# Optimization experiments

Measured on AMD Instinct MI355X. Metric: run time of the kernel, lower is better.

## Reference

```python
import jax, jax.numpy as jnp
import numpy as np

# dims (match init_kwargs / input_specs)
D = 768      # embed_dim
H = 12       # num query heads
G = 4        # num kv groups
E = 8        # num experts
K = 2        # experts per token
F = 4 * D    # ffn hidden dim
B, S, T = 2, 1024, 1024
DH = D // H  # head dim = 64
EPS = 1e-6


def setup_inputs() -> dict:
    key = jax.random.key(0)
    ks = jax.random.split(key, 16)

    def p(k, shape, scale=0.02):
        return jax.random.normal(k, shape, jnp.float32) * scale

    inp = {}
    inp['x'] = jax.random.normal(ks[0], (B, S, D), jnp.float32)
    inp['encoder_context'] = jax.random.normal(ks[1], (B, T, D), jnp.float32)
    for n in ('ln1', 'ln2', 'ln3'):
        inp[n + '_scale'] = jnp.ones((D,), jnp.float32)
        inp[n + '_bias'] = jnp.zeros((D,), jnp.float32)
    i = 2
    for pre in ('sa', 'ca'):
        inp[pre + '_wq'] = p(ks[i], (D, H * DH)); i += 1
        inp[pre + '_bq'] = jnp.zeros((H * DH,), jnp.float32)
        inp[pre + '_wk'] = p(ks[i], (D, G * DH)); i += 1
        inp[pre + '_bk'] = jnp.zeros((G * DH,), jnp.float32)
        inp[pre + '_wv'] = p(ks[i], (D, G * DH)); i += 1
        inp[pre + '_bv'] = jnp.zeros((G * DH,), jnp.float32)
        inp[pre + '_wo'] = p(ks[i], (H * DH, D)); i += 1
        inp[pre + '_bo'] = jnp.zeros((D,), jnp.float32)
    inp['gate_w'] = p(ks[i], (D, E)); i += 1
    inp['gate_b'] = jnp.zeros((E,), jnp.float32)
    inp['w1'] = p(ks[i], (E, D, F)); i += 1
    inp['b1'] = jnp.zeros((E, F), jnp.float32)
    inp['w2'] = p(ks[i], (E, F, D)); i += 1
    inp['b2'] = jnp.zeros((E, D), jnp.float32)
    return inp


def _ln(x, scale, bias):
    mu = jnp.mean(x, axis=-1, keepdims=True)
    var = jnp.mean(jnp.square(x - mu), axis=-1, keepdims=True)
    return (x - mu) * jax.lax.rsqrt(var + EPS) * scale + bias


def _gqa(q_in, kv_in, wq, bq, wk, bk, wv, bv, wo, bo, causal):
    Bq, Sq, _ = q_in.shape
    Skv = kv_in.shape[1]
    q = (q_in @ wq + bq).reshape(Bq, Sq, H, DH)
    k = (kv_in @ wk + bk).reshape(Bq, Skv, G, DH)
    v = (kv_in @ wv + bv).reshape(Bq, Skv, G, DH)
    rep = H // G
    k = jnp.repeat(k, rep, axis=2)  # [B,Skv,H,DH]
    v = jnp.repeat(v, rep, axis=2)
    scores = jnp.einsum('bqhd,bkhd->bhqk', q, k) / jnp.sqrt(jnp.asarray(DH, q.dtype))
    if causal:
        cmask = jnp.tril(jnp.ones((Sq, Skv), bool))
        scores = jnp.where(cmask[None, None], scores, jnp.finfo(scores.dtype).min)
    attn = jax.nn.softmax(scores, axis=-1)
    out = jnp.einsum('bhqk,bkhd->bqhd', attn, v).reshape(Bq, Sq, H * DH)
    return out @ wo + bo


def _moe(x, gate_w, gate_b, w1, b1, w2, b2):
    logits = x @ gate_w + gate_b                      # [B,S,E]
    probs = jax.nn.softmax(logits, axis=-1)
    top_v, top_i = jax.lax.top_k(probs, K)            # [B,S,K]
    top_v = top_v / jnp.sum(top_v, axis=-1, keepdims=True)
    combine = jnp.sum(jax.nn.one_hot(top_i, E, dtype=x.dtype) * top_v[..., None], axis=-2)  # [B,S,E]
    h = jax.nn.gelu(jnp.einsum('bsd,edf->ebsf', x, w1) + b1[:, None, None, :])
    y = jnp.einsum('ebsf,efd->ebsd', h, w2) + b2[:, None, None, :]
    return jnp.einsum('ebsd,bse->bsd', y, combine)


def reference(x, encoder_context,
              ln1_scale, ln1_bias, ln2_scale, ln2_bias, ln3_scale, ln3_bias,
              sa_wq, sa_bq, sa_wk, sa_bk, sa_wv, sa_bv, sa_wo, sa_bo,
              ca_wq, ca_bq, ca_wk, ca_bk, ca_wv, ca_bv, ca_wo, ca_bo,
              gate_w, gate_b, w1, b1, w2, b2):
    xn = _ln(x, ln1_scale, ln1_bias)
    x = x + _gqa(xn, xn, sa_wq, sa_bq, sa_wk, sa_bk, sa_wv, sa_bv, sa_wo, sa_bo, causal=True)
    xn = _ln(x, ln2_scale, ln2_bias)
    x = x + _gqa(xn, encoder_context, ca_wq, ca_bq, ca_wk, ca_bk, ca_wv, ca_bv, ca_wo, ca_bo, causal=False)
    xn = _ln(x, ln3_scale, ln3_bias)
    x = x + _moe(xn, gate_w, gate_b, w1, b1, w2, b2)
    return x
```

## Files before the change

### kernel.cpp

```cpp
#include <hip/hip_runtime.h>

#define DEV __device__ __forceinline__

typedef __attribute__((ext_vector_type(4))) float f32x4;
typedef __attribute__((ext_vector_type(8))) short short8;
typedef __attribute__((ext_vector_type(4))) unsigned int u32x4;
typedef __attribute__((ext_vector_type(4))) unsigned short us16x4;

#define D_ 768
#define S_ 1024
#define B_ 2
#define H_ 12
#define G_ 4
#define DH_ 64
#define E_ 8
#define F_ 3072
#define NTOK (B_*S_)

DEV unsigned short f2bf(float f){
  unsigned int b = __float_as_uint(f);
  b += 0x7FFFu + ((b >> 16) & 1u);
  return (unsigned short)(b >> 16);
}
DEV float bf2f(unsigned short h){ return __uint_as_float(((unsigned int)h) << 16); }
DEV unsigned int splitbf_pack(float v){
  unsigned short h = f2bf(v);
  unsigned short l = f2bf(v - bf2f(h));
  return (unsigned int)h | ((unsigned int)l << 16);
}

__global__ __launch_bounds__(256) void tcast_kernel(const float* __restrict__ W,
                                                    unsigned short* __restrict__ Wh,
                                                    unsigned short* __restrict__ Wl,
                                                    int K, int N){
  __shared__ float tile[32][33];
  long long zoff = (long long)blockIdx.z * K * N;
  const float* Wz = W + zoff;
  int n0 = blockIdx.x*32, k0 = blockIdx.y*32;
  int tx = threadIdx.x, ty = threadIdx.y;
  #pragma unroll
  for (int i=0;i<4;i++){
    int r = ty + i*8;
    tile[r][tx] = Wz[(long long)(k0+r)*N + n0 + tx];
  }
  __syncthreads();
  #pragma unroll
  for (int i=0;i<4;i++){
    int r = ty + i*8;
    float v = tile[tx][r];
    unsigned int hl = splitbf_pack(v);
    long long o = zoff + (long long)(n0+r)*K + k0 + tx;
    Wh[o] = (unsigned short)(hl & 0xFFFFu);
    if (Wl) Wl[o] = (unsigned short)(hl >> 16);
  }
}

__global__ __launch_bounds__(256) void ln_kernel(const float* __restrict__ x,
                                                 const float* __restrict__ sc,
                                                 const float* __restrict__ bi,
                                                 unsigned short* __restrict__ outb,
                                                 float* __restrict__ outf){
  __shared__ float red[8];
  long long row = blockIdx.x;
  const float* xr = x + row*D_;
  int tid = threadIdx.x;
  float v0 = xr[tid], v1 = xr[tid+256], v2 = xr[tid+512];
  float s = v0+v1+v2;
  float q = v0*v0 + v1*v1 + v2*v2;
  #pragma unroll
  for (int off=32; off; off>>=1){ s += __shfl_xor(s, off); q += __shfl_xor(q, off); }
  int lane = tid & 63, w = tid >> 6;
  if (lane == 0){ red[w] = s; red[4+w] = q; }
  __syncthreads();
  s = red[0]+red[1]+red[2]+red[3];
  q = red[4]+red[5]+red[6]+red[7];
  float mu  = s * (1.0f/D_);
  float var = q * (1.0f/D_) - mu*mu;
  float rstd = rsqrtf(var + 1e-6f);
  #pragma unroll
  for (int i=0;i<3;i++){
    int idx = tid + 256*i;
    float vv = (i==0) ? v0 : (i==1) ? v1 : v2;
    float o = (vv - mu)*rstd*sc[idx] + bi[idx];
    outf[row*D_ + idx] = o;
    if (outb) outb[row*D_ + idx] = f2bf(o);
  }
}

#define LDK 80
__global__ __launch_bounds__(256) void gemm_split(
    const float* __restrict__ A, int lda,
    const unsigned short* __restrict__ Wh,
    const unsigned short* __restrict__ Wl,
    const float* __restrict__ bias,
    const float* __restrict__ resid,
    float* __restrict__ Cf, int ldc,
    int K)
{
  __shared__ __align__(16) unsigned short Ash[64*LDK];
  __shared__ __align__(16) unsigned short Asl[64*LDK];
  __shared__ __align__(16) unsigned short Bsh[64*LDK];
  __shared__ __align__(16) unsigned short Bsl[64*LDK];
  const int r0 = blockIdx.y*64;
  const int n0 = blockIdx.x*64;
  const int tid = threadIdx.x;
  const int lane = tid & 63;
  const int wv = tid >> 6;
  const int wr = (wv>>1)*32, wc = (wv&1)*32;

  f32x4 acc[2][2];
  #pragma unroll
  for (int i=0;i<2;i++)
    #pragma unroll
    for (int j=0;j<2;j++) acc[i][j] = (f32x4){0.f,0.f,0.f,0.f};

  for (int k0 = 0; k0 < K; k0 += 64){
    #pragma unroll
    for (int i=0;i<2;i++){
      int c = tid + i*256;
      int rr = c >> 3;
      int kc = (c & 7) * 8;
      const float* ap = A + (long long)(r0+rr)*lda + k0 + kc;
      f32x4 a0 = *(const f32x4*)(ap);
      f32x4 a1 = *(const f32x4*)(ap + 4);
      unsigned int p0 = splitbf_pack(a0.x), p1 = splitbf_pack(a0.y);
      unsigned int p2 = splitbf_pack(a0.z), p3 = splitbf_pack(a0.w);
      unsigned int p4 = splitbf_pack(a1.x), p5 = splitbf_pack(a1.y);
      unsigned int p6 = splitbf_pack(a1.z), p7 = splitbf_pack(a1.w);
      us16x4 h0, h1, l0, l1;
      h0.x=(unsigned short)p0; l0.x=(unsigned short)(p0>>16);
      h0.y=(unsigned short)p1; l0.y=(unsigned short)(p1>>16);
      h0.z=(unsigned short)p2; l0.z=(unsigned short)(p2>>16);
      h0.w=(unsigned short)p3; l0.w=(unsigned short)(p3>>16);
      h1.x=(unsigned short)p4; l1.x=(unsigned short)(p4>>16);
      h1.y=(unsigned short)p5; l1.y=(unsigned short)(p5>>16);
      h1.z=(unsigned short)p6; l1.z=(unsigned short)(p6>>16);
      h1.w=(unsigned short)p7; l1.w=(unsigned short)(p7>>16);
      *(us16x4*)&Ash[rr*LDK + kc]     = h0;
      *(us16x4*)&Ash[rr*LDK + kc + 4] = h1;
      *(us16x4*)&Asl[rr*LDK + kc]     = l0;
      *(us16x4*)&Asl[rr*LDK + kc + 4] = l1;
      long long bo = (long long)(n0+rr)*K + k0 + kc;
      *(u32x4*)&Bsh[rr*LDK + kc] = *(const u32x4*)(Wh + bo);
      *(u32x4*)&Bsl[rr*LDK + kc] = *(const u32x4*)(Wl + bo);
    }
    __syncthreads();
    #pragma unroll
    for (int ks=0; ks<2; ks++){
      int koff = ks*32 + (lane>>4)*8;
      short8 ah0 = *(const short8*)&Ash[(wr +      (lane&15))*LDK + koff];
      short8 ah1 = *(const short8*)&Ash[(wr + 16 + (lane&15))*LDK + koff];
      short8 al0 = *(const short8*)&Asl[(wr +      (lane&15))*LDK + koff];
      short8 al1 = *(const short8*)&Asl[(wr + 16 + (lane&15))*LDK + koff];
      short8 bh0 = *(const short8*)&Bsh[(wc +      (lane&15))*LDK + koff];
      short8 bh1 = *(const short8*)&Bsh[(wc + 16 + (lane&15))*LDK + koff];
      short8 bl0 = *(const short8*)&Bsl[(wc +      (lane&15))*LDK + koff];
      short8 bl1 = *(const short8*)&Bsl[(wc + 16 + (lane&15))*LDK + koff];
      acc[0][0] = __builtin_amdgcn_mfma_f32_16x16x32_bf16(ah0, bh0, acc[0][0], 0,0,0);
      acc[0][1] = __builtin_amdgcn_mfma_f32_16x16x32_bf16(ah0, bh1, acc[0][1], 0,0,0);
      acc[1][0] = __builtin_amdgcn_mfma_f32_16x16x32_bf16(ah1, bh0, acc[1][0], 0,0,0);
      acc[1][1] = __builtin_amdgcn_mfma_f32_16x16x32_bf16(ah1, bh1, acc[1][1], 0,0,0);
      acc[0][0] = __builtin_amdgcn_mfma_f32_16x16x32_bf16(ah0, bl0, acc[0][0], 0,0,0);
      acc[0][1] = __builtin_amdgcn_mfma_f32_16x16x32_bf16(ah0, bl1, acc[0][1], 0,0,0);
      acc[1][0] = __builtin_amdgcn_mfma_f32_16x16x32_bf16(ah1, bl0, acc[1][0], 0,0,0);
      acc[1][1] = __builtin_amdgcn_mfma_f32_16x16x32_bf16(ah1, bl1, acc[1][1], 0,0,0);
      acc[0][0] = __builtin_amdgcn_mfma_f32_16x16x32_bf16(al0, bh0, acc[0][0], 0,0,0);
      acc[0][1] = __builtin_amdgcn_mfma_f32_16x16x32_bf16(al0, bh1, acc[0][1], 0,0,0);
      acc[1][0] = __builtin_amdgcn_mfma_f32_16x16x32_bf16(al1, bh0, acc[1][0], 0,0,0);
      acc[1][1] = __builtin_amdgcn_mfma_f32_16x16x32_bf16(al1, bh1, acc[1][1], 0,0,0);
    }
    __syncthreads();
  }

  #pragma unroll
  for (int fi=0; fi<2; fi++)
  #pragma unroll
  for (int fj=0; fj<2; fj++)
  #pragma unroll
  for (int reg=0; reg<4; reg++){
    int r = r0 + wr + fi*16 + (lane>>4)*4 + reg;
    int col = n0 + wc + fj*16 + (lane&15);
    float val = acc[fi][fj][reg] + bias[col];
    if (resid) val += resid[(long long)r*ldc + col];
    Cf[(long long)r*ldc + col] = val;
  }
}

__global__ __launch_bounds__(256) void gemm_nt(
    const unsigned short* __restrict__ A, int lda,
    const unsigned short* __restrict__ Wt, long long wstride,
    const float* __restrict__ bias, int bias_stride,
    const int* __restrict__ counts,
    const int* __restrict__ a_idx, int a_idx_stride,
    const int* __restrict__ row_base,
    float* __restrict__ Cf, unsigned short* __restrict__ Cb, int ldc,
    int M, int K, int do_gelu)
{
  __shared__ __align__(16) unsigned short As[64*LDK];
  __shared__ __align__(16) unsigned short Bs[64*LDK];
  const int z = blockIdx.z;
  const int Mz = counts ? counts[z] : M;
  const int r0 = blockIdx.y*64;
  if (r0 >= Mz) return;
  const int n0 = blockIdx.x*64;
  const int obase = row_base ? row_base[z] : 0;
  const unsigned short* Wz = Wt + (long long)z*wstride;
  const float* bz = bias + (long long)z*bias_stride;
  const int tid = threadIdx.x;
  const int lane = tid & 63;
  const int wv = tid >> 6;
  const int wr = (wv>>1)*32, wc = (wv&1)*32;

  long long arow[2];
  #pragma unroll
  for (int i=0;i<2;i++){
    int c = tid + i*256;
    int rr = c >> 3;
    int r = r0 + rr;
    int rcl = (r < Mz) ? r : (Mz-1);
    arow[i] = a_idx ? (long long)a_idx[(long long)z*a_idx_stride + rcl]
                    : (long long)(obase + rcl);
  }

  f32x4 acc[2][2];
  #pragma unroll
  for (int i=0;i<2;i++)
    #pragma unroll
    for (int j=0;j<2;j++) acc[i][j] = (f32x4){0.f,0.f,0.f,0.f};

  for (int k0 = 0; k0 < K; k0 += 64){
    #pragma unroll
    for (int i=0;i<2;i++){
      int c = tid + i*256;
      int rr = c >> 3;
      int kc = (c & 7) * 8;
      *(u32x4*)&As[rr*LDK + kc] = *(const u32x4*)(A + arow[i]*lda + k0 + kc);
      *(u32x4*)&Bs[rr*LDK + kc] = *(const u32x4*)(Wz + (long long)(n0+rr)*K + k0 + kc);
    }
    __syncthreads();
    #pragma unroll
    for (int ks=0; ks<2; ks++){
      int koff = ks*32 + (lane>>4)*8;
      short8 a0 = *(const short8*)&As[(wr +      (lane&15))*LDK + koff];
      short8 a1 = *(const short8*)&As[(wr + 16 + (lane&15))*LDK + koff];
      short8 b0 = *(const short8*)&Bs[(wc +      (lane&15))*LDK + koff];
      short8 b1 = *(const short8*)&Bs[(wc + 16 + (lane&15))*LDK + koff];
      acc[0][0] = __builtin_amdgcn_mfma_f32_16x16x32_bf16(a0, b0, acc[0][0], 0,0,0);
      acc[0][1] = __builtin_amdgcn_mfma_f32_16x16x32_bf16(a0, b1, acc[0][1], 0,0,0);
      acc[1][0] = __builtin_amdgcn_mfma_f32_16x16x32_bf16(a1, b0, acc[1][0], 0,0,0);
      acc[1][1] = __builtin_amdgcn_mfma_f32_16x16x32_bf16(a1, b1, acc[1][1], 0,0,0);
    }
    __syncthreads();
  }

  #pragma unroll
  for (int fi=0; fi<2; fi++)
  #pragma unroll
  for (int fj=0; fj<2; fj++)
  #pragma unroll
  for (int reg=0; reg<4; reg++){
    int ml = wr + fi*16 + (lane>>4)*4 + reg;
    int r = r0 + ml;
    if (r >= Mz) continue;
    int col = n0 + wc + fj*16 + (lane&15);
    float val = acc[fi][fj][reg] + bz[col];
    if (do_gelu){
      float xx = val;
      float t = tanhf(0.7978845608028654f*(xx + 0.044715f*xx*xx*xx));
      val = 0.5f*xx*(1.0f + t);
    }
    long long orow = (long long)obase + r;
    if (Cf) Cf[orow*ldc + col] = val;
    if (Cb) Cb[orow*ldc + col] = f2bf(val);
  }
}

__global__ __launch_bounds__(256) void kv_split_kernel(const float* __restrict__ in,
                                                       unsigned short* __restrict__ hi,
                                                       unsigned short* __restrict__ lo,
                                                       int n4){
  int i = blockIdx.x*256 + threadIdx.x;
  if (i >= n4) return;
  f32x4 v = *(const f32x4*)(in + (long long)i*4);
  unsigned int p0 = splitbf_pack(v.x), p1 = splitbf_pack(v.y);
  unsigned int p2 = splitbf_pack(v.z), p3 = splitbf_pack(v.w);
  us16x4 h, l;
  h.x=(unsigned short)p0; l.x=(unsigned short)(p0>>16);
  h.y=(unsigned short)p1; l.y=(unsigned short)(p1>>16);
  h.z=(unsigned short)p2; l.z=(unsigned short)(p2>>16);
  h.w=(unsigned short)p3; l.w=(unsigned short)(p3>>16);
  *(us16x4*)(hi + (long long)i*4) = h;
  *(us16x4*)(lo + (long long)i*4) = l;
}

__global__ __launch_bounds__(256) void vt_split_kernel(const float* __restrict__ vin,
                                                       unsigned short* __restrict__ vth,
                                                       unsigned short* __restrict__ vtl){
  __shared__ float tile[32][33];
  int s0 = blockIdx.x*32, d0 = blockIdx.y*32;
  int bg = blockIdx.z; int b = bg >> 2, g = bg & 3;
  int tx = threadIdx.x, ty = threadIdx.y;
  #pragma unroll
  for (int i=0;i<4;i++){
    int r = ty + i*8;
    tile[r][tx] = vin[(long long)(b*1024 + s0 + r)*256 + g*64 + d0 + tx];
  }
  __syncthreads();
  #pragma unroll
  for (int i=0;i<4;i++){
    int d = d0 + ty + i*8;
    unsigned int pk = splitbf_pack(tile[tx][ty + i*8]);
    long long o = (long long)(bg*64 + d)*1024 + s0 + tx;
    vth[o] = (unsigned short)(pk & 0xFFFFu);
    vtl[o] = (unsigned short)(pk >> 16);
  }
}

#define AT_LDK 72
#define AT_LDP 76
__global__ __launch_bounds__(256, 2) void attn_mfma(
    const float* __restrict__ q,
    const unsigned short* __restrict__ kh, const unsigned short* __restrict__ kl,
    const unsigned short* __restrict__ vth, const unsigned short* __restrict__ vtl,
    float* __restrict__ ctx, int causal)
{
  __shared__ __align__(16) unsigned short KhS[64*AT_LDK];
  __shared__ __align__(16) unsigned short KlS[64*AT_LDK];
  __shared__ __align__(16) unsigned short VhS[64*AT_LDK];
  __shared__ __align__(16) unsigned short VlS[64*AT_LDK];
  __shared__ __align__(16) unsigned int   Pp[4][16*AT_LDP];

  const int qblk = blockIdx.x;
  const int h = blockIdx.y;
  const int b = blockIdx.z;
  const int g = h / (H_/G_);
  const int tid = threadIdx.x;
  const int lane = tid & 63;
  const int w = tid >> 6;
  const int l15 = lane & 15;
  const int l4 = lane >> 4;
  const int qb0 = qblk*64;

  short8 qh[2], ql[2];
  #pragma unroll
  for (int ks=0; ks<2; ks++){
    const float* qp = q + ((long long)(b*S_ + qb0 + w*16 + l15))*D_ + h*DH_ + ks*32 + l4*8;
    f32x4 q0 = *(const f32x4*)qp;
    f32x4 q1 = *(const f32x4*)(qp + 4);
    float qq[8] = {q0.x,q0.y,q0.z,q0.w,q1.x,q1.y,q1.z,q1.w};
    #pragma unroll
    for (int j=0;j<8;j++){
      unsigned int pk = splitbf_pack(qq[j]*0.125f);
      qh[ks][j] = (short)(pk & 0xFFFFu);
      ql[ks][j] = (short)(pk >> 16);
    }
  }

  f32x4 o[4];
  #pragma unroll
  for (int fd=0; fd<4; fd++) o[fd] = (f32x4){0.f,0.f,0.f,0.f};
  float m[4]    = {-3.0e38f,-3.0e38f,-3.0e38f,-3.0e38f};
  float lsum[4] = {0.f,0.f,0.f,0.f};

  const int ntiles = causal ? (qblk + 1) : (S_/64);
  for (int kt=0; kt<ntiles; kt++){
    __syncthreads();
    {
      int r = tid >> 2, c = tid & 3;
      long long krow = (long long)(b*S_ + kt*64 + r)*(G_*DH_) + g*DH_;
      long long vrow = (long long)((b*G_ + g)*64 + r)*S_ + kt*64;
      *(u32x4*)&KhS[r*AT_LDK + c*8]     = *(const u32x4*)(kh + krow + c*8);
      *(u32x4*)&KhS[r*AT_LDK + (c+4)*8] = *(const u32x4*)(kh + krow + (c+4)*8);
      *(u32x4*)&KlS[r*AT_LDK + c*8]     = *(const u32x4*)(kl + krow + c*8);
      *(u32x4*)&KlS[r*AT_LDK + (c+4)*8] = *(const u32x4*)(kl + krow + (c+4)*8);
      *(u32x4*)&VhS[r*AT_LDK + c*8]     = *(const u32x4*)(vth + vrow + c*8);
      *(u32x4*)&VhS[r*AT_LDK + (c+4)*8] = *(const u32x4*)(vth + vrow + (c+4)*8);
      *(u32x4*)&VlS[r*AT_LDK + c*8]     = *(const u32x4*)(vtl + vrow + c*8);
      *(u32x4*)&VlS[r*AT_LDK + (c+4)*8] = *(const u32x4*)(vtl + vrow + (c+4)*8);
    }
// ... 56 lines not shown
      ps += __shfl_xor(ps, 4); ps += __shfl_xor(ps, 8);
      lsum[reg] = lsum[reg]*c[reg] + ps;
      o[0][reg] *= c[reg]; o[1][reg] *= c[reg];
      o[2][reg] *= c[reg]; o[3][reg] *= c[reg];
    }

    #pragma unroll
    for (int ks=0; ks<2; ks++){
      u32x4 pa = *(const u32x4*)&Pp[w][l15*AT_LDP + ks*32 + l4*8];
      u32x4 pb = *(const u32x4*)&Pp[w][l15*AT_LDP + ks*32 + l4*8 + 4];
      short8 ph, pl;
      #pragma unroll
      for (int j=0;j<4;j++){
        ph[j]   = (short)(pa[j] & 0xFFFFu); pl[j]   = (short)(pa[j] >> 16);
        ph[4+j] = (short)(pb[j] & 0xFFFFu); pl[4+j] = (short)(pb[j] >> 16);
      }
      #pragma unroll
      for (int fd=0; fd<4; fd++){
        short8 vh = *(const short8*)&VhS[(fd*16 + l15)*AT_LDK + ks*32 + l4*8];
        short8 vl = *(const short8*)&VlS[(fd*16 + l15)*AT_LDK + ks*32 + l4*8];
        o[fd] = __builtin_amdgcn_mfma_f32_16x16x32_bf16(ph, vh, o[fd], 0,0,0);
        o[fd] = __builtin_amdgcn_mfma_f32_16x16x32_bf16(pl, vh, o[fd], 0,0,0);
        o[fd] = __builtin_amdgcn_mfma_f32_16x16x32_bf16(ph, vl, o[fd], 0,0,0);
      }
    }
  }

  #pragma unroll
  for (int reg=0; reg<4; reg++){
    float inv = 1.0f / lsum[reg];
    long long tok = b*S_ + qb0 + w*16 + l4*4 + reg;
    #pragma unroll
    for (int fd=0; fd<4; fd++){
      ctx[tok*D_ + h*DH_ + fd*16 + l15] = o[fd][reg]*inv;
    }
  }
}

__global__ __launch_bounds__(256) void gate_kernel(const float* __restrict__ xnf,
                                                   const float* __restrict__ gw,
                                                   const float* __restrict__ gb,
                                                   int* __restrict__ counts,
                                                   int* __restrict__ toklist,
                                                   int* __restrict__ route_e,
                                                   int* __restrict__ route_pos,
                                                   float* __restrict__ route_w){
  int t = blockIdx.x*4 + (threadIdx.x >> 6);
  int lane = threadIdx.x & 63;
  float acc[E_];
  #pragma unroll
  for (int e=0;e<E_;e++) acc[e] = 0.f;
  #pragma unroll
  for (int i=0;i<12;i++){
    int d = lane + 64*i;
    float xv = xnf[(long long)t*D_ + d];
    const float* w = gw + (long long)d*E_;
    #pragma unroll
    for (int e=0;e<E_;e++) acc[e] += xv*w[e];
  }
  #pragma unroll
  for (int off=32; off; off>>=1)
    #pragma unroll
    for (int e=0;e<E_;e++) acc[e] += __shfl_xor(acc[e], off);
  if (lane == 0){
    #pragma unroll
    for (int e=0;e<E_;e++) acc[e] += gb[e];
    int e0 = 0;
// ... 53 lines not shown
  const float* ln2b  = (const float*)d_in[5];
  const float* ln3s  = (const float*)d_in[6];
  const float* ln3b  = (const float*)d_in[7];
  const float* sa_wq = (const float*)d_in[8];
  const float* sa_bq = (const float*)d_in[9];
  const float* sa_wk = (const float*)d_in[10];
  const float* sa_bk = (const float*)d_in[11];
  const float* sa_wv = (const float*)d_in[12];
  const float* sa_bv = (const float*)d_in[13];
  const float* sa_wo = (const float*)d_in[14];
  const float* sa_bo = (const float*)d_in[15];
  const float* ca_wq = (const float*)d_in[16];
  const float* ca_bq = (const float*)d_in[17];
  const float* ca_wk = (const float*)d_in[18];
  const float* ca_bk = (const float*)d_in[19];
  const float* ca_wv = (const float*)d_in[20];
  const float* ca_bv = (const float*)d_in[21];
  const float* ca_wo = (const float*)d_in[22];
  const float* ca_bo = (const float*)d_in[23];
  const float* gate_w= (const float*)d_in[24];
  const float* gate_b= (const float*)d_in[25];
  const float* w1    = (const float*)d_in[26];
  const float* b1    = (const float*)d_in[27];
  const float* w2    = (const float*)d_in[28];
  const float* b2    = (const float*)d_in[29];
  float* out = (float*)d_out;

  char* p = (char*)d_ws;
  auto alloc = [&](size_t bytes)->void*{
    void* r = (void*)p;
    p += (bytes + 255) & ~(size_t)255;
    return r;
  };
  unsigned short* wqh_sa = (unsigned short*)alloc((size_t)D_*D_*2);
  unsigned short* wql_sa = (unsigned short*)alloc((size_t)D_*D_*2);
  unsigned short* wkh_sa = (unsigned short*)alloc((size_t)D_*G_*DH_*2);
  unsigned short* wkl_sa = (unsigned short*)alloc((size_t)D_*G_*DH_*2);
  unsigned short* wvh_sa = (unsigned short*)alloc((size_t)D_*G_*DH_*2);
  unsigned short* wvl_sa = (unsigned short*)alloc((size_t)D_*G_*DH_*2);
  unsigned short* woh_sa = (unsigned short*)alloc((size_t)D_*D_*2);
  unsigned short* wol_sa = (unsigned short*)alloc((size_t)D_*D_*2);
  unsigned short* wqh_ca = (unsigned short*)alloc((size_t)D_*D_*2);
  unsigned short* wql_ca = (unsigned short*)alloc((size_t)D_*D_*2);
  unsigned short* wkh_ca = (unsigned short*)alloc((size_t)D_*G_*DH_*2);
  unsigned short* wkl_ca = (unsigned short*)alloc((size_t)D_*G_*DH_*2);
  unsigned short* wvh_ca = (unsigned short*)alloc((size_t)D_*G_*DH_*2);
  unsigned short* wvl_ca = (unsigned short*)alloc((size_t)D_*G_*DH_*2);
  unsigned short* woh_ca = (unsigned short*)alloc((size_t)D_*D_*2);
  unsigned short* wol_ca = (unsigned short*)alloc((size_t)D_*D_*2);
  unsigned short* w1T = (unsigned short*)alloc((size_t)E_*D_*F_*2);
  unsigned short* w2T = (unsigned short*)alloc((size_t)E_*D_*F_*2);
  unsigned short* xn_b = (unsigned short*)alloc((size_t)NTOK*D_*2);
  unsigned short* hbuf = (unsigned short*)alloc((size_t)2*NTOK*F_*2);
  unsigned short* khp = (unsigned short*)alloc((size_t)NTOK*G_*DH_*2);
  unsigned short* klp = (unsigned short*)alloc((size_t)NTOK*G_*DH_*2);
  unsigned short* vtp_h = (unsigned short*)alloc((size_t)NTOK*G_*DH_*2);
  unsigned short* vtp_l = (unsigned short*)alloc((size_t)NTOK*G_*DH_*2);
  float* xnf  = (float*)alloc((size_t)NTOK*D_*4);
  float* qbuf = (float*)alloc((size_t)NTOK*D_*4);
  float* kbuf = (float*)alloc((size_t)NTOK*G_*DH_*4);
  float* vbuf = (float*)alloc((size_t)NTOK*G_*DH_*4);
  float* ctx  = (float*)alloc((size_t)NTOK*D_*4);
  float* xbuf = (float*)alloc((size_t)NTOK*D_*4);
  float* ybuf = (float*)alloc((size_t)2*NTOK*D_*4);
  int* counts    = (int*)alloc(E_*4);
  int* offs      = (int*)alloc(E_*4);
  int* toklist   = (int*)alloc((size_t)E_*NTOK*4);
  int* route_e   = (int*)alloc((size_t)2*NTOK*4);
  int* route_pos = (int*)alloc((size_t)2*NTOK*4);
  float* route_w = (float*)alloc((size_t)2*NTOK*4);

  (void)hipMemsetAsync(counts, 0, E_*sizeof(int), stream);

  dim3 tb(32,8);
  tcast_kernel<<<dim3(24,24,1), tb, 0, stream>>>(sa_wq, wqh_sa, wql_sa, 768, 768);
  tcast_kernel<<<dim3( 8,24,1), tb, 0, stream>>>(sa_wk, wkh_sa, wkl_sa, 768, 256);
  tcast_kernel<<<dim3( 8,24,1), tb, 0, stream>>>(sa_wv, wvh_sa, wvl_sa, 768, 256);
  tcast_kernel<<<dim3(24,24,1), tb, 0, stream>>>(sa_wo, woh_sa, wol_sa, 768, 768);
  tcast_kernel<<<dim3(24,24,1), tb, 0, stream>>>(ca_wq, wqh_ca, wql_ca, 768, 768);
  tcast_kernel<<<dim3( 8,24,1), tb, 0, stream>>>(ca_wk, wkh_ca, wkl_ca, 768, 256);
  tcast_kernel<<<dim3( 8,24,1), tb, 0, stream>>>(ca_wv, wvh_ca, wvl_ca, 768, 256);
  tcast_kernel<<<dim3(24,24,1), tb, 0, stream>>>(ca_wo, woh_ca, wol_ca, 768, 768);
  tcast_kernel<<<dim3(96,24,E_), tb, 0, stream>>>(w1, w1T, nullptr, 768, 3072);
  tcast_kernel<<<dim3(24,96,E_), tb, 0, stream>>>(w2, w2T, nullptr, 3072, 768);

  ln_kernel<<<NTOK, 256, 0, stream>>>(x, ln1s, ln1b, nullptr, xnf);
  gemm_split<<<dim3(12,32), 256, 0, stream>>>(xnf, 768, wqh_sa, wql_sa, sa_bq, nullptr, qbuf, 768, 768);
  gemm_split<<<dim3( 4,32), 256, 0, stream>>>(xnf, 768, wkh_sa, wkl_sa, sa_bk, nullptr, kbuf, 256, 768);
  gemm_split<<<dim3( 4,32), 256, 0, stream>>>(xnf, 768, wvh_sa, wvl_sa, sa_bv, nullptr, vbuf, 256, 768);
  kv_split_kernel<<<dim3(NTOK*G_*DH_/4/256), 256, 0, stream>>>(kbuf, khp, klp, NTOK*G_*DH_/4);
  vt_split_kernel<<<dim3(32,2,8), tb, 0, stream>>>(vbuf, vtp_h, vtp_l);
  attn_mfma<<<dim3(16,12,2), 256, 0, stream>>>(qbuf, khp, klp, vtp_h, vtp_l, ctx, 1);
  gemm_split<<<dim3(12,32), 256, 0, stream>>>(ctx, 768, woh_sa, wol_sa, sa_bo, x, xbuf, 768, 768);

  ln_kernel<<<NTOK, 256, 0, stream>>>(xbuf, ln2s, ln2b, nullptr, xnf);
  gemm_split<<<dim3(12,32), 256, 0, stream>>>(xnf, 768, wqh_ca, wql_ca, ca_bq, nullptr, qbuf, 768, 768);
  gemm_split<<<dim3( 4,32), 256, 0, stream>>>(enc, 768, wkh_ca, wkl_ca, ca_bk, nullptr, kbuf, 256, 768);
  gemm_split<<<dim3( 4,32), 256, 0, stream>>>(enc, 768, wvh_ca, wvl_ca, ca_bv, nullptr, vbuf, 256, 768);
  kv_split_kernel<<<dim3(NTOK*G_*DH_/4/256), 256, 0, stream>>>(kbuf, khp, klp, NTOK*G_*DH_/4);
  vt_split_kernel<<<dim3(32,2,8), tb, 0, stream>>>(vbuf, vtp_h, vtp_l);
  attn_mfma<<<dim3(16,12,2), 256, 0, stream>>>(qbuf, khp, klp, vtp_h, vtp_l, ctx, 0);
  gemm_split<<<dim3(12,32), 256, 0, stream>>>(ctx, 768, woh_ca, wol_ca, ca_bo, xbuf, xbuf, 768, 768);

  ln_kernel<<<NTOK, 256, 0, stream>>>(xbuf, ln3s, ln3b, xn_b, xnf);
  gate_kernel<<<NTOK/4, 256, 0, stream>>>(xnf, gate_w, gate_b,
      counts, toklist, route_e, route_pos, route_w);
  offsets_kernel<<<1, 64, 0, stream>>>(counts, offs);
  gemm_nt<<<dim3(48,32,E_), 256, 0, stream>>>(xn_b, 768, w1T, (long long)F_*D_, b1, F_,
      counts, toklist, NTOK, offs, nullptr, hbuf, F_, NTOK, 768, 1);
  gemm_nt<<<dim3(12,32,E_), 256, 0, stream>>>(hbuf, F_, w2T, (long long)F_*D_, b2, D_,
      counts, nullptr, 0, offs, ybuf, nullptr, 768, NTOK, F_, 0);
  combine_kernel<<<NTOK, 192, 0, stream>>>(xbuf, ybuf, route_e, route_pos, route_w, offs, out);
}
```

Measured before the change: 537.3 us.

## Fuse QKV projections, pre-split activations, and enlarge GEMM tiles to 128

Concatenates the self-attention Q/K/V weights and the cross-attention K/V weights so each group is one GEMM launch. LayerNorm and attention now emit hi/lo bf16 splits directly, so the GEMMs load pre-split operands instead of converting fp32 in the inner loop. The split GEMM tiles grow to 128 rows and the MoE GEMMs to 128x128, which raises reuse per load but lowers block count and occupancy. Several conversion kernels are removed, and a few small bias-concat and encoder-split kernels are added.

```diff
diff --git a/kernel.cpp b/kernel.cpp
--- a/kernel.cpp
+++ b/kernel.cpp
@@ -55,10 +55,37 @@
   }
 }
 
+__global__ void split_rows(const float* __restrict__ in, int ld, int width,
+                           unsigned short* __restrict__ hi, unsigned short* __restrict__ lo){
+  long long t = blockIdx.x;
+  int c = threadIdx.x*4;
+  f32x4 v = *(const f32x4*)(in + t*ld + c);
+  unsigned int p0 = splitbf_pack(v.x), p1 = splitbf_pack(v.y);
+  unsigned int p2 = splitbf_pack(v.z), p3 = splitbf_pack(v.w);
+  us16x4 h, l;
+  h.x=(unsigned short)p0; l.x=(unsigned short)(p0>>16);
+  h.y=(unsigned short)p1; l.y=(unsigned short)(p1>>16);
+  h.z=(unsigned short)p2; l.z=(unsigned short)(p2>>16);
+  h.w=(unsigned short)p3; l.w=(unsigned short)(p3>>16);
+  *(us16x4*)(hi + t*width + c) = h;
+  *(us16x4*)(lo + t*width + c) = l;
+}
+
+__global__ void concat_bias(const float* __restrict__ b0, int n0,
+                            const float* __restrict__ b1, int n1,
+                            const float* __restrict__ b2, int n2,
+                            float* __restrict__ out){
+  int i = blockIdx.x*256 + threadIdx.x;
+  if (i < n0) out[i] = b0[i];
+  else if (i < n0+n1) out[i] = b1[i-n0];
+  else if (i < n0+n1+n2) out[i] = b2[i-n0-n1];
+}
+
 __global__ __launch_bounds__(256) void ln_kernel(const float* __restrict__ x,
                                                  const float* __restrict__ sc,
                                                  const float* __restrict__ bi,
-                                                 unsigned short* __restrict__ outb,
+                                                 unsigned short* __restrict__ outh,
+                                                 unsigned short* __restrict__ outl,
                                                  float* __restrict__ outf){
   __shared__ float red[8];
   long long row = blockIdx.x;
@@ -82,111 +109,96 @@
     int idx = tid + 256*i;
     float vv = (i==0) ? v0 : (i==1) ? v1 : v2;
     float o = (vv - mu)*rstd*sc[idx] + bi[idx];
-    outf[row*D_ + idx] = o;
-    if (outb) outb[row*D_ + idx] = f2bf(o);
+    unsigned int pk = splitbf_pack(o);
+    outh[row*D_ + idx] = (unsigned short)(pk & 0xFFFFu);
+    if (outl) outl[row*D_ + idx] = (unsigned short)(pk >> 16);
+    if (outf) outf[row*D_ + idx] = o;
   }
 }
 
 #define LDK 80
-__global__ __launch_bounds__(256) void gemm_split(
-    const float* __restrict__ A, int lda,
-    const unsigned short* __restrict__ Wh,
-    const unsigned short* __restrict__ Wl,
+__global__ __launch_bounds__(256) void gemm3(
+    const unsigned short* __restrict__ Ah, const unsigned short* __restrict__ Al, int lda,
+    const unsigned short* __restrict__ Wh, const unsigned short* __restrict__ Wl, int K,
     const float* __restrict__ bias,
-    const float* __restrict__ resid,
-    float* __restrict__ Cf, int ldc,
-    int K)
+    const float* __restrict__ resid, int ldr,
+    float* __restrict__ Cf, int ldc)
 {
-  __shared__ __align__(16) unsigned short Ash[64*LDK];
-  __shared__ __align__(16) unsigned short Asl[64*LDK];
-  __shared__ __align__(16) unsigned short Bsh[64*LDK];
-  __shared__ __align__(16) unsigned short Bsl[64*LDK];
-  const int r0 = blockIdx.y*64;
+  __shared__ __align__(16) unsigned short AshH[128*LDK];
+  __shared__ __align__(16) unsigned short AshL[128*LDK];
+  __shared__ __align__(16) unsigned short BshH[64*LDK];
+  __shared__ __align__(16) unsigned short BshL[64*LDK];
+  const int r0 = blockIdx.y*128;
   const int n0 = blockIdx.x*64;
   const int tid = threadIdx.x;
   const int lane = tid & 63;
   const int wv = tid >> 6;
-  const int wr = (wv>>1)*32, wc = (wv&1)*32;
-
-  f32x4 acc[2][2];
-  #pragma unroll
-  for (int i=0;i<2;i++)
+  const int wr = (wv>>1)*64, wc = (wv&1)*32;
+  const int l15 = lane & 15, l4 = lane >> 4;
+
+  f32x4 acc[4][2];
+  #pragma unroll
+  for (int i=0;i<4;i++)
     #pragma unroll
     for (int j=0;j<2;j++) acc[i][j] = (f32x4){0.f,0.f,0.f,0.f};
 
   for (int k0 = 0; k0 < K; k0 += 64){
+    #pragma unroll
+    for (int i=0;i<4;i++){
+      int c = tid + i*256;
+      int rr = c >> 3, kc = (c & 7)*8;
+      long long src = (long long)(r0+rr)*lda + k0 + kc;
+      *(u32x4*)&AshH[rr*LDK+kc] = *(const u32x4*)(Ah + src);
+      *(u32x4*)&AshL[rr*LDK+kc] = *(const u32x4*)(Al + src);
+    }
     #pragma unroll
     for (int i=0;i<2;i++){
       int c = tid + i*256;
-      int rr = c >> 3;
-      int kc = (c & 7) * 8;
-      const float* ap = A + (long long)(r0+rr)*lda + k0 + kc;
-      f32x4 a0 = *(const f32x4*)(ap);
-      f32x4 a1 = *(const f32x4*)(ap + 4);
-      unsigned int p0 = splitbf_pack(a0.x), p1 = splitbf_pack(a0.y);
-      unsigned int p2 = splitbf_pack(a0.z), p3 = splitbf_pack(a0.w);
-      unsigned int p4 = splitbf_pack(a1.x), p5 = splitbf_pack(a1.y);
-      unsigned int p6 = splitbf_pack(a1.z), p7 = splitbf_pack(a1.w);
-      us16x4 h0, h1, l0, l1;
-      h0.x=(unsigned short)p0; l0.x=(unsigned short)(p0>>16);
-      h0.y=(unsigned short)p1; l0.y=(unsigned short)(p1>>16);
-      h0.z=(unsigned short)p2; l0.z=(unsigned short)(p2>>16);
-      h0.w=(unsigned short)p3; l0.w=(unsigned short)(p3>>16);
-      h1.x=(unsigned short)p4; l1.x=(unsigned short)(p4>>16);
-      h1.y=(unsigned short)p5; l1.y=(unsigned short)(p5>>16);
-      h1.z=(unsigned short)p6; l1.z=(unsigned short)(p6>>16);
-      h1.w=(unsigned short)p7; l1.w=(unsigned short)(p7>>16);
-      *(us16x4*)&Ash[rr*LDK + kc]     = h0;
-      *(us16x4*)&Ash[rr*LDK + kc + 4] = h1;
-      *(us16x4*)&Asl[rr*LDK + kc]     = l0;
-      *(us16x4*)&Asl[rr*LDK + kc + 4] = l1;
-      long long bo = (long long)(n0+rr)*K + k0 + kc;
-      *(u32x4*)&Bsh[rr*LDK + kc] = *(const u32x4*)(Wh + bo);
-      *(u32x4*)&Bsl[rr*LDK + kc] = *(const u32x4*)(Wl + bo);
+      int rr = c >> 3, kc = (c & 7)*8;
+      long long src = (long long)(n0+rr)*K + k0 + kc;
+      *(u32x4*)&BshH[rr*LDK+kc] = *(const u32x4*)(Wh + src);
+      *(u32x4*)&BshL[rr*LDK+kc] = *(const u32x4*)(Wl + src);
     }
     __syncthreads();
     #pragma unroll
     for (int ks=0; ks<2; ks++){
-      int koff = ks*32 + (lane>>4)*8;
-      short8 ah0 = *(const short8*)&Ash[(wr +      (lane&15))*LDK + koff];
-      short8 ah1 = *(const short8*)&Ash[(wr + 16 + (lane&15))*LDK + koff];
-      short8 al0 = *(const short8*)&Asl[(wr +      (lane&15))*LDK + koff];
-      short8 al1 = *(const short8*)&Asl[(wr + 16 + (lane&15))*LDK + koff];
-      short8 bh0 = *(const short8*)&Bsh[(wc +      (lane&15))*LDK + koff];
-      short8 bh1 = *(const short8*)&Bsh[(wc + 16 + (lane&15))*LDK + koff];
-      short8 bl0 = *(const short8*)&Bsl[(wc +      (lane&15))*LDK + koff];
-      short8 bl1 = *(const short8*)&Bsl[(wc + 16 + (lane&15))*LDK + koff];
-      acc[0][0] = __builtin_amdgcn_mfma_f32_16x16x32_bf16(ah0, bh0, acc[0][0], 0,0,0);
-      acc[0][1] = __builtin_amdgcn_mfma_f32_16x16x32_bf16(ah0, bh1, acc[0][1], 0,0,0);
-      acc[1][0] = __builtin_amdgcn_mfma_f32_16x16x32_bf16(ah1, bh0, acc[1][0], 0,0,0);
-      acc[1][1] = __builtin_amdgcn_mfma_f32_16x16x32_bf16(ah1, bh1, acc[1][1], 0,0,0);
-      acc[0][0] = __builtin_amdgcn_mfma_f32_16x16x32_bf16(ah0, bl0, acc[0][0], 0,0,0);
-      acc[0][1] = __builtin_amdgcn_mfma_f32_16x16x32_bf16(ah0, bl1, acc[0][1], 0,0,0);
-      acc[1][0] = __builtin_amdgcn_mfma_f32_16x16x32_bf16(ah1, bl0, acc[1][0], 0,0,0);
-      acc[1][1] = __builtin_amdgcn_mfma_f32_16x16x32_bf16(ah1, bl1, acc[1][1], 0,0,0);
-      acc[0][0] = __builtin_amdgcn_mfma_f32_16x16x32_bf16(al0, bh0, acc[0][0], 0,0,0);
-      acc[0][1] = __builtin_amdgcn_mfma_f32_16x16x32_bf16(al0, bh1, acc[0][1], 0,0,0);
-      acc[1][0] = __builtin_amdgcn_mfma_f32_16x16x32_bf16(al1, bh0, acc[1][0], 0,0,0);
-      acc[1][1] = __builtin_amdgcn_mfma_f32_16x16x32_bf16(al1, bh1, acc[1][1], 0,0,0);
+      int koff = ks*32 + l4*8;
+      short8 bh[2], bl[2];
+      #pragma unroll
+      for (int fj=0; fj<2; fj++){
+        bh[fj] = *(const short8*)&BshH[(wc + fj*16 + l15)*LDK + koff];
+        bl[fj] = *(const short8*)&BshL[(wc + fj*16 + l15)*LDK + koff];
+      }
+      #pragma unroll
+      for (int fi=0; fi<4; fi++){
+        short8 ah = *(const short8*)&AshH[(wr + fi*16 + l15)*LDK + koff];
+        short8 al = *(const short8*)&AshL[(wr + fi*16 + l15)*LDK + koff];
+        #pragma unroll
+        for (int fj=0; fj<2; fj++){
+          acc[fi][fj] = __builtin_amdgcn_mfma_f32_16x16x32_bf16(ah, bh[fj], acc[fi][fj], 0,0,0);
+          acc[fi][fj] = __builtin_amdgcn_mfma_f32_16x16x32_bf16(al, bh[fj], acc[fi][fj], 0,0,0);
+          acc[fi][fj] = __builtin_amdgcn_mfma_f32_16x16x32_bf16(ah, bl[fj], acc[fi][fj], 0,0,0);
+        }
+      }
     }
     __syncthreads();
   }
 
   #pragma unroll
-  for (int fi=0; fi<2; fi++)
+  for (int fi=0; fi<4; fi++)
   #pragma unroll
   for (int fj=0; fj<2; fj++)
   #pragma unroll
   for (int reg=0; reg<4; reg++){
-    int r = r0 + wr + fi*16 + (lane>>4)*4 + reg;
-    int col = n0 + wc + fj*16 + (lane&15);
+    int r = r0 + wr + fi*16 + l4*4 + reg;
+    int col = n0 + wc + fj*16 + l15;
     float val = acc[fi][fj][reg] + bias[col];
-    if (resid) val += resid[(long long)r*ldc + col];
+    if (resid) val += resid[(long long)r*ldr + col];
     Cf[(long long)r*ldc + col] = val;
   }
 }
 
-__global__ __launch_bounds__(256) void gemm_nt(
+__global__ __launch_bounds__(256) void gemm_nt128(
     const unsigned short* __restrict__ A, int lda,
     const unsigned short* __restrict__ Wt, long long wstride,
     const float* __restrict__ bias, int bias_stride,
@@ -194,26 +206,27 @@
     const int* __restrict__ a_idx, int a_idx_stride,
     const int* __restrict__ row_base,
     float* __restrict__ Cf, unsigned short* __restrict__ Cb, int ldc,
-    int M, int K, int do_gelu)
+    int K, int do_gelu)
 {
-  __shared__ __align__(16) unsigned short As[64*LDK];
-  __shared__ __align__(16) unsigned short Bs[64*LDK];
+  __shared__ __align__(16) unsigned short As[128*LDK];
+  __shared__ __align__(16) unsigned short Bs[128*LDK];
   const int z = blockIdx.z;
-  const int Mz = counts ? counts[z] : M;
-  const int r0 = blockIdx.y*64;
+  const int Mz = counts[z];
+  const int r0 = blockIdx.y*128;
   if (r0 >= Mz) return;
-  const int n0 = blockIdx.x*64;
-  const int obase = row_base ? row_base[z] : 0;
+  const int n0 = blockIdx.x*128;
+  const int obase = row_base[z];
   const unsigned short* Wz = Wt + (long long)z*wstride;
   const float* bz = bias + (long long)z*bias_stride;
   const int tid = threadIdx.x;
   const int lane = tid & 63;
   const int wv = tid >> 6;
-  const int wr = (wv>>1)*32, wc = (wv&1)*32;
-
-  long long arow[2];
-  #pragma unroll
-  for (int i=0;i<2;i++){
+  const int wr = (wv>>1)*64, wc = (wv&1)*64;
+  const int l15 = lane & 15, l4 = lane >> 4;
+
+  long long arow[4];
+  #pragma unroll
+  for (int i=0;i<4;i++){
     int c = tid + i*256;
     int rr = c >> 3;
     int r = r0 + rr;
@@ -222,47 +235,48 @@
                     : (long long)(obase + rcl);
   }
 
-  f32x4 acc[2][2];
-  #pragma unroll
-  for (int i=0;i<2;i++)
-    #pragma unroll
-    for (int j=0;j<2;j++) acc[i][j] = (f32x4){0.f,0.f,0.f,0.f};
+  f32x4 acc[4][4];
+  #pragma unroll
+  for (int i=0;i<4;i++)
+    #pragma unroll
+    for (int j=0;j<4;j++) acc[i][j] = (f32x4){0.f,0.f,0.f,0.f};
 
   for (int k0 = 0; k0 < K; k0 += 64){
     #pragma unroll
-    for (int i=0;i<2;i++){
+    for (int i=0;i<4;i++){
       int c = tid + i*256;
-      int rr = c >> 3;
-      int kc = (c & 7) * 8;
-      *(u32x4*)&As[rr*LDK + kc] = *(const u32x4*)(A + arow[i]*lda + k0 + kc);
-      *(u32x4*)&Bs[rr*LDK + kc] = *(const u32x4*)(Wz + (long long)(n0+rr)*K + k0 + kc);
+      int rr = c >> 3, kc = (c & 7)*8;
+      *(u32x4*)&As[rr*LDK+kc] = *(const u32x4*)(A + arow[i]*lda + k0 + kc);
+      *(u32x4*)&Bs[rr*LDK+kc] = *(const u32x4*)(Wz + (long long)(n0+rr)*K + k0 + kc);
     }
     __syncthreads();
     #pragma unroll
     for (int ks=0; ks<2; ks++){
-      int koff = ks*32 + (lane>>4)*8;
-      short8 a0 = *(const short8*)&As[(wr +      (lane&15))*LDK + koff];
-      short8 a1 = *(const short8*)&As[(wr + 16 + (lane&15))*LDK + koff];
-      short8 b0 = *(const short8*)&Bs[(wc +      (lane&15))*LDK + koff];
-      short8 b1 = *(const short8*)&Bs[(wc + 16 + (lane&15))*LDK + koff];
-      acc[0][0] = __builtin_amdgcn_mfma_f32_16x16x32_bf16(a0, b0, acc[0][0], 0,0,0);
-      acc[0][1] = __builtin_amdgcn_mfma_f32_16x16x32_bf16(a0, b1, acc[0][1], 0,0,0);
-      acc[1][0] = __builtin_amdgcn_mfma_f32_16x16x32_bf16(a1, b0, acc[1][0], 0,0,0);
-      acc[1][1] = __builtin_amdgcn_mfma_f32_16x16x32_bf16(a1, b1, acc[1][1], 0,0,0);
+      int koff = ks*32 + l4*8;
+      short8 a[4], b[4];
+      #pragma unroll
+      for (int f=0; f<4; f++){
+        a[f] = *(const short8*)&As[(wr + f*16 + l15)*LDK + koff];
+        b[f] = *(const short8*)&Bs[(wc + f*16 + l15)*LDK + koff];
+      }
+      #pragma unroll
+      for (int fi=0; fi<4; fi++)
+        #pragma unroll
+        for (int fj=0; fj<4; fj++)
+          acc[fi][fj] = __builtin_amdgcn_mfma_f32_16x16x32_bf16(a[fi], b[fj], acc[fi][fj], 0,0,0);
     }
     __syncthreads();
   }
 
   #pragma unroll
-  for (int fi=0; fi<2; fi++)
-  #pragma unroll
-  for (int fj=0; fj<2; fj++)
+  for (int fi=0; fi<4; fi++)
+  #pragma unroll
+  for (int fj=0; fj<4; fj++)
   #pragma unroll
   for (int reg=0; reg<4; reg++){
-    int ml = wr + fi*16 + (lane>>4)*4 + reg;
-    int r = r0 + ml;
+    int r = r0 + wr + fi*16 + l4*4 + reg;
     if (r >= Mz) continue;
-    int col = n0 + wc + fj*16 + (lane&15);
+    int col = n0 + wc + fj*16 + l15;
     float val = acc[fi][fj][reg] + bz[col];
     if (do_gelu){
       float xx = val;
@@ -275,25 +289,8 @@
   }
 }
 
-__global__ __launch_bounds__(256) void kv_split_kernel(const float* __restrict__ in,
-                                                       unsigned short* __restrict__ hi,
-                                                       unsigned short* __restrict__ lo,
-                                                       int n4){
-  int i = blockIdx.x*256 + threadIdx.x;
-  if (i >= n4) return;
-  f32x4 v = *(const f32x4*)(in + (long long)i*4);
-  unsigned int p0 = splitbf_pack(v.x), p1 = splitbf_pack(v.y);
-  unsigned int p2 = splitbf_pack(v.z), p3 = splitbf_pack(v.w);
-  us16x4 h, l;
-  h.x=(unsigned short)p0; l.x=(unsigned short)(p0>>16);
-  h.y=(unsigned short)p1; l.y=(unsigned short)(p1>>16);
-  h.z=(unsigned short)p2; l.z=(unsigned short)(p2>>16);
-  h.w=(unsigned short)p3; l.w=(unsigned short)(p3>>16);
-  *(us16x4*)(hi + (long long)i*4) = h;
-  *(us16x4*)(lo + (long long)i*4) = l;
-}
-
 __global__ __launch_bounds__(256) void vt_split_kernel(const float* __restrict__ vin,
+                                                       int ld, int cofs,
                                                        unsigned short* __restrict__ vth,
                                                        unsigned short* __restrict__ vtl){
   __shared__ float tile[32][33];
@@ -303,7 +300,7 @@
   #pragma unroll
   for (int i=0;i<4;i++){
     int r = ty + i*8;
-    tile[r][tx] = vin[(long long)(b*1024 + s0 + r)*256 + g*64 + d0 + tx];
+    tile[r][tx] = vin[(long long)(b*1024 + s0 + r)*ld + cofs + g*64 + d0 + tx];
   }
   __syncthreads();
   #pragma unroll
@@ -319,10 +316,10 @@
 #define AT_LDK 72
 #define AT_LDP 76
 __global__ __launch_bounds__(256, 2) void attn_mfma(
-    const float* __restrict__ q,
+    const float* __restrict__ q, int qld,
     const unsigned short* __restrict__ kh, const unsigned short* __restrict__ kl,
     const unsigned short* __restrict__ vth, const unsigned short* __restrict__ vtl,
-    float* __restrict__ ctx, int causal)
+    unsigned short* __restrict__ ctxh, unsigned short* __restrict__ ctxl, int causal)
 {
   __shared__ __align__(16) unsigned short KhS[64*AT_LDK];
   __shared__ __align__(16) unsigned short KlS[64*AT_LDK];
@@ -344,7 +341,7 @@
   short8 qh[2], ql[2];
   #pragma unroll
   for (int ks=0; ks<2; ks++){
-    const float* qp = q + ((long long)(b*S_ + qb0 + w*16 + l15))*D_ + h*DH_ + ks*32 + l4*8;
+    const float* qp = q + ((long long)(b*S_ + qb0 + w*16 + l15))*qld + h*DH_ + ks*32 + l4*8;
     f32x4 q0 = *(const f32x4*)qp;
     f32x4 q1 = *(const f32x4*)(qp + 4);
     float qq[8] = {q0.x,q0.y,q0.z,q0.w,q1.x,q1.y,q1.z,q1.w};
@@ -467,7 +464,10 @@
     long long tok = b*S_ + qb0 + w*16 + l4*4 + reg;
     #pragma unroll
     for (int fd=0; fd<4; fd++){
-      ctx[tok*D_ + h*DH_ + fd*16 + l15] = o[fd][reg]*inv;
+      unsigned int pk = splitbf_pack(o[fd][reg]*inv);
+      long long oidx = tok*D_ + h*DH_ + fd*16 + l15;
+      ctxh[oidx] = (unsigned short)(pk & 0xFFFFu);
+      ctxl[oidx] = (unsigned short)(pk >> 16);
     }
   }
 }
@@ -587,35 +587,34 @@
     p += (bytes + 255) & ~(size_t)255;
     return r;
   };
-  unsigned short* wqh_sa = (unsigned short*)alloc((size_t)D_*D_*2);
-  unsigned short* wql_sa = (unsigned short*)alloc((size_t)D_*D_*2);
-  unsigned short* wkh_sa = (unsigned short*)alloc((size_t)D_*G_*DH_*2);
-  unsigned short* wkl_sa = (unsigned short*)alloc((size_t)D_*G_*DH_*2);
-  unsigned short* wvh_sa = (unsigned short*)alloc((size_t)D_*G_*DH_*2);
-  unsigned short* wvl_sa = (unsigned short*)alloc((size_t)D_*G_*DH_*2);
-  unsigned short* woh_sa = (unsigned short*)alloc((size_t)D_*D_*2);
-  unsigned short* wol_sa = (unsigned short*)alloc((size_t)D_*D_*2);
-  unsigned short* wqh_ca = (unsigned short*)alloc((size_t)D_*D_*2);
-  unsigned short* wql_ca = (unsigned short*)alloc((size_t)D_*D_*2);
-  unsigned short* wkh_ca = (unsigned short*)alloc((size_t)D_*G_*DH_*2);
-  unsigned short* wkl_ca = (unsigned short*)alloc((size_t)D_*G_*DH_*2);
-  unsigned short* wvh_ca = (unsigned short*)alloc((size_t)D_*G_*DH_*2);
-  unsigned short* wvl_ca = (unsigned short*)alloc((size_t)D_*G_*DH_*2);
-  unsigned short* woh_ca = (unsigned short*)alloc((size_t)D_*D_*2);
-  unsigned short* wol_ca = (unsigned short*)alloc((size_t)D_*D_*2);
+  unsigned short* wqkvh_sa = (unsigned short*)alloc((size_t)1280*768*2);
+  unsigned short* wqkvl_sa = (unsigned short*)alloc((size_t)1280*768*2);
+  unsigned short* woh_sa   = (unsigned short*)alloc((size_t)768*768*2);
+  unsigned short* wol_sa   = (unsigned short*)alloc((size_t)768*768*2);
+  unsigned short* wqh_ca   = (unsigned short*)alloc((size_t)768*768*2);
+  unsigned short* wql_ca   = (unsigned short*)alloc((size_t)768*768*2);
+  unsigned short* wkvh_ca  = (unsigned short*)alloc((size_t)512*768*2);
+  unsigned short* wkvl_ca  = (unsigned short*)alloc((size_t)512*768*2);
+  unsigned short* woh_ca   = (unsigned short*)alloc((size_t)768*768*2);
+  unsigned short* wol_ca   = (unsigned short*)alloc((size_t)768*768*2);
   unsigned short* w1T = (unsigned short*)alloc((size_t)E_*D_*F_*2);
   unsigned short* w2T = (unsigned short*)alloc((size_t)E_*D_*F_*2);
+  float* bqkv_sa = (float*)alloc(1280*4);
+  float* bkv_ca  = (float*)alloc(512*4);
+  unsigned short* ench = (unsigned short*)alloc((size_t)NTOK*D_*2);
+  unsigned short* encl = (unsigned short*)alloc((size_t)NTOK*D_*2);
+  unsigned short* xh   = (unsigned short*)alloc((size_t)NTOK*D_*2);
+  unsigned short* xl   = (unsigned short*)alloc((size_t)NTOK*D_*2);
+  unsigned short* ctxh = (unsigned short*)alloc((size_t)NTOK*D_*2);
+  unsigned short* ctxl = (unsigned short*)alloc((size_t)NTOK*D_*2);
   unsigned short* xn_b = (unsigned short*)alloc((size_t)NTOK*D_*2);
   unsigned short* hbuf = (unsigned short*)alloc((size_t)2*NTOK*F_*2);
-  unsigned short* khp = (unsigned short*)alloc((size_t)NTOK*G_*DH_*2);
-  unsigned short* klp = (unsigned short*)alloc((size_t)NTOK*G_*DH_*2);
+  unsigned short* khp   = (unsigned short*)alloc((size_t)NTOK*G_*DH_*2);
+  unsigned short* klp   = (unsigned short*)alloc((size_t)NTOK*G_*DH_*2);
   unsigned short* vtp_h = (unsigned short*)alloc((size_t)NTOK*G_*DH_*2);
   unsigned short* vtp_l = (unsigned short*)alloc((size_t)NTOK*G_*DH_*2);
+  float* qkvbuf = (float*)alloc((size_t)NTOK*1280*4);
   float* xnf  = (float*)alloc((size_t)NTOK*D_*4);
-  float* qbuf = (float*)alloc((size_t)NTOK*D_*4);
-  float* kbuf = (float*)alloc((size_t)NTOK*G_*DH_*4);
-  float* vbuf = (float*)alloc((size_t)NTOK*G_*DH_*4);
-  float* ctx  = (float*)alloc((size_t)NTOK*D_*4);
   float* xbuf = (float*)alloc((size_t)NTOK*D_*4);
   float* ybuf = (float*)alloc((size_t)2*NTOK*D_*4);
   int* counts    = (int*)alloc(E_*4);
@@ -628,42 +627,47 @@
   (void)hipMemsetAsync(counts, 0, E_*sizeof(int), stream);
 
   dim3 tb(32,8);
-  tcast_kernel<<<dim3(24,24,1), tb, 0, stream>>>(sa_wq, wqh_sa, wql_sa, 768, 768);
-  tcast_kernel<<<dim3( 8,24,1), tb, 0, stream>>>(sa_wk, wkh_sa, wkl_sa, 768, 256);
-  tcast_kernel<<<dim3( 8,24,1), tb, 0, stream>>>(sa_wv, wvh_sa, wvl_sa, 768, 256);
+  tcast_kernel<<<dim3(24,24,1), tb, 0, stream>>>(sa_wq, wqkvh_sa,            wqkvl_sa,            768, 768);
+  tcast_kernel<<<dim3( 8,24,1), tb, 0, stream>>>(sa_wk, wqkvh_sa + 768*768,  wqkvl_sa + 768*768,  768, 256);
+  tcast_kernel<<<dim3( 8,24,1), tb, 0, stream>>>(sa_wv, wqkvh_sa + 1024*768, wqkvl_sa + 1024*768, 768, 256);
   tcast_kernel<<<dim3(24,24,1), tb, 0, stream>>>(sa_wo, woh_sa, wol_sa, 768, 768);
   tcast_kernel<<<dim3(24,24,1), tb, 0, stream>>>(ca_wq, wqh_ca, wql_ca, 768, 768);
-  tcast_kernel<<<dim3( 8,24,1), tb, 0, stream>>>(ca_wk, wkh_ca, wkl_ca, 768, 256);
-  tcast_kernel<<<dim3( 8,24,1), tb, 0, stream>>>(ca_wv, wvh_ca, wvl_ca, 768, 256);
+  tcast_kernel<<<dim3( 8,24,1), tb, 0, stream>>>(ca_wk, wkvh_ca,           wkvl_ca,           768, 256);
+  tcast_kernel<<<dim3( 8,24,1), tb, 0, stream>>>(ca_wv, wkvh_ca + 256*768, wkvl_ca + 256*768, 768, 256);
   tcast_kernel<<<dim3(24,24,1), tb, 0, stream>>>(ca_wo, woh_ca, wol_ca, 768, 768);
   tcast_kernel<<<dim3(96,24,E_), tb, 0, stream>>>(w1, w1T, nullptr, 768, 3072);
   tcast_kernel<<<dim3(24,96,E_), tb, 0, stream>>>(w2, w2T, nullptr, 3072, 768);
-
-  ln_kernel<<<NTOK, 256, 0, stream>>>(x, ln1s, ln1b, nullptr, xnf);
-  gemm_split<<<dim3(12,32), 256, 0, stream>>>(xnf, 768, wqh_sa, wql_sa, sa_bq, nullptr, qbuf, 768, 768);
-  gemm_split<<<dim3( 4,32), 256, 0, stream>>>(xnf, 768, wkh_sa, wkl_sa, sa_bk, nullptr, kbuf, 256, 768);
-  gemm_split<<<dim3( 4,32), 256, 0, stream>>>(xnf, 768, wvh_sa, wvl_sa, sa_bv, nullptr, vbuf, 256, 768);
-  kv_split_kernel<<<dim3(NTOK*G_*DH_/4/256), 256, 0, stream>>>(kbuf, khp, klp, NTOK*G_*DH_/4);
-  vt_split_kernel<<<dim3(32,2,8), tb, 0, stream>>>(vbuf, vtp_h, vtp_l);
-  attn_mfma<<<dim3(16,12,2), 256, 0, stream>>>(qbuf, khp, klp, vtp_h, vtp_l, ctx, 1);
-  gemm_split<<<dim3(12,32), 256, 0, stream>>>(ctx, 768, woh_sa, wol_sa, sa_bo, x, xbuf, 768, 768);
-
-  ln_kernel<<<NTOK, 256, 0, stream>>>(xbuf, ln2s, ln2b, nullptr, xnf);
-  gemm_split<<<dim3(12,32), 256, 0, stream>>>(xnf, 768, wqh_ca, wql_ca, ca_bq, nullptr, qbuf, 768, 768);
-  gemm_split<<<dim3( 4,32), 256, 0, stream>>>(enc, 768, wkh_ca, wkl_ca, ca_bk, nullptr, kbuf, 256, 768);
-  gemm_split<<<dim3( 4,32), 256, 0, stream>>>(enc, 768, wvh_ca, wvl_ca, ca_bv, nullptr, vbuf, 256, 768);
-  kv_split_kernel<<<dim3(NTOK*G_*DH_/4/256), 256, 0, stream>>>(kbuf, khp, klp, NTOK*G_*DH_/4);
-  vt_split_kernel<<<dim3(32,2,8), tb, 0, stream>>>(vbuf, vtp_h, vtp_l);
-  attn_mfma<<<dim3(16,12,2), 256, 0, stream>>>(qbuf, khp, klp, vtp_h, vtp_l, ctx, 0);
-  gemm_split<<<dim3(12,32), 256, 0, stream>>>(ctx, 768, woh_ca, wol_ca, ca_bo, xbuf, xbuf, 768, 768);
-
-  ln_kernel<<<NTOK, 256, 0, stream>>>(xbuf, ln3s, ln3b, xn_b, xnf);
+  concat_bias<<<5, 256, 0, stream>>>(sa_bq, 768, sa_bk, 256, sa_bv, 256, bqkv_sa);
+  concat_bias<<<2, 256, 0, stream>>>(ca_bk, 256, ca_bv, 256, nullptr, 0, bkv_ca);
+  split_rows<<<NTOK, 192, 0, stream>>>(enc, 768, 768, ench, encl);
+
+  ln_kernel<<<NTOK, 256, 0, stream>>>(x, ln1s, ln1b, xh, xl, nullptr);
+  gemm3<<<dim3(20,16), 256, 0, stream>>>(xh, xl, 768, wqkvh_sa, wqkvl_sa, 768,
+      bqkv_sa, nullptr, 0, qkvbuf, 1280);
+  split_rows<<<NTOK, 64, 0, stream>>>(qkvbuf + 768, 1280, 256, khp, klp);
+  vt_split_kernel<<<dim3(32,2,8), tb, 0, stream>>>(qkvbuf, 1280, 1024, vtp_h, vtp_l);
+  attn_mfma<<<dim3(16,12,2), 256, 0, stream>>>(qkvbuf, 1280, khp, klp, vtp_h, vtp_l, ctxh, ctxl, 1);
+  gemm3<<<dim3(12,16), 256, 0, stream>>>(ctxh, ctxl, 768, woh_sa, wol_sa, 768,
+      sa_bo, x, 768, xbuf, 768);
+
+  ln_kernel<<<NTOK, 256, 0, stream>>>(xbuf, ln2s, ln2b, xh, xl, nullptr);
+  gemm3<<<dim3(12,16), 256, 0, stream>>>(xh, xl, 768, wqh_ca, wql_ca, 768,
+      ca_bq, nullptr, 0, qkvbuf, 1280);
+  gemm3<<<dim3(8,16), 256, 0, stream>>>(ench, encl, 768, wkvh_ca, wkvl_ca, 768,
+      bkv_ca, nullptr, 0, qkvbuf + 768, 1280);
+  split_rows<<<NTOK, 64, 0, stream>>>(qkvbuf + 768, 1280, 256, khp, klp);
+  vt_split_kernel<<<dim3(32,2,8), tb, 0, stream>>>(qkvbuf, 1280, 1024, vtp_h, vtp_l);
+  attn_mfma<<<dim3(16,12,2), 256, 0, stream>>>(qkvbuf, 1280, khp, klp, vtp_h, vtp_l, ctxh, ctxl, 0);
+  gemm3<<<dim3(12,16), 256, 0, stream>>>(ctxh, ctxl, 768, woh_ca, wol_ca, 768,
+      ca_bo, xbuf, 768, xbuf, 768);
+
+  ln_kernel<<<NTOK, 256, 0, stream>>>(xbuf, ln3s, ln3b, xn_b, nullptr, xnf);
   gate_kernel<<<NTOK/4, 256, 0, stream>>>(xnf, gate_w, gate_b,
       counts, toklist, route_e, route_pos, route_w);
   offsets_kernel<<<1, 64, 0, stream>>>(counts, offs);
-  gemm_nt<<<dim3(48,32,E_), 256, 0, stream>>>(xn_b, 768, w1T, (long long)F_*D_, b1, F_,
-      counts, toklist, NTOK, offs, nullptr, hbuf, F_, NTOK, 768, 1);
-  gemm_nt<<<dim3(12,32,E_), 256, 0, stream>>>(hbuf, F_, w2T, (long long)F_*D_, b2, D_,
-      counts, nullptr, 0, offs, ybuf, nullptr, 768, NTOK, F_, 0);
+  gemm_nt128<<<dim3(24,16,E_), 256, 0, stream>>>(xn_b, 768, w1T, (long long)F_*D_, b1, F_,
+      counts, toklist, NTOK, offs, nullptr, hbuf, F_, 768, 1);
+  gemm_nt128<<<dim3(6,16,E_), 256, 0, stream>>>(hbuf, F_, w2T, (long long)F_*D_, b2, D_,
+      counts, nullptr, 0, offs, ybuf, nullptr, 768, F_, 0);
   combine_kernel<<<NTOK, 192, 0, stream>>>(xbuf, ybuf, route_e, route_pos, route_w, offs, out);
 }
```

Result: no change. 539.7 us (+0.4%).
